# Optimization experiments

Hardware: AMD Instinct MI355X
Metric: run time of the kernel (lower is better)

Reference implementation:

```python
import jax, jax.numpy as jnp
import numpy as np

N = 50000
E = 600000
F_IN = 256
H = 128            # num_hidden_units * num_heads (heads=1)
C = 20             # num_classes
NEG_SLOPE = 0.2    # PyG GATConv default


def setup_inputs() -> dict:
    key = jax.random.key(0)
    ks = jax.random.split(key, 16)
    g = lambda k, shape, fan: jax.random.normal(k, shape, jnp.float32) / np.sqrt(fan)
    return {
        "x": jax.random.normal(ks[0], (N, F_IN), jnp.float32),
        "edge_index": jax.random.randint(ks[1], (2, E), 0, N, jnp.int64),
        # GATConv 1: F_IN -> H (heads=1, concat)
        "W1": g(ks[2], (F_IN, H), F_IN),
        "a_src1": g(ks[3], (H,), H),
        "a_dst1": g(ks[4], (H,), H),
        "b1": jnp.zeros((H,), jnp.float32),
        # GATConv 2: H -> H (heads=1)
        "W2": g(ks[5], (H, H), H),
        "a_src2": g(ks[6], (H,), H),
        "a_dst2": g(ks[7], (H,), H),
        "b2": jnp.zeros((H,), jnp.float32),
        # MLP head
        "Wm1": g(ks[8], (H, H), H),
        "bm1": jnp.zeros((H,), jnp.float32),
        "Wm2": g(ks[9], (H, C), H),
        "bm2": jnp.zeros((C,), jnp.float32),
    }


def gat_layer(x, W, a_src, a_dst, b, src, dst, n_nodes):
    """Single-head GATConv (PyG semantics, self-loops already in src/dst)."""
    h = x @ W                                    # [N, H]
    # edge attention logits: leaky_relu(a_src . h_j + a_dst . h_i)
    logits = jax.nn.leaky_relu((h @ a_src)[src] + (h @ a_dst)[dst], NEG_SLOPE)  # [Etot]
    # softmax over incoming edges per target node
    m = jax.ops.segment_max(logits, dst, num_segments=n_nodes)
    e = jnp.exp(logits - m[dst])
    denom = jax.ops.segment_sum(e, dst, num_segments=n_nodes)
    coef = e / denom[dst]                        # [Etot]
    out = jax.ops.segment_sum(coef[:, None] * h[src], dst, num_segments=n_nodes)
    return out + b


def reference(x, edge_index, W1, a_src1, a_dst1, b1, W2, a_src2, a_dst2, b2, Wm1, bm1, Wm2, bm2):
    n = x.shape[0]
    loops = jnp.arange(n, dtype=edge_index.dtype)
    src = jnp.concatenate([edge_index[0], loops])  # add self loops (GATConv default)
    dst = jnp.concatenate([edge_index[1], loops])
    h = gat_layer(x, W1, a_src1, a_dst1, b1, src, dst, n)
    h = jax.nn.relu(h)                            # dropout = identity at eval
    h = gat_layer(h, W2, a_src2, a_dst2, b2, src, dst, n)
    # MLP head: Linear -> (dropout) -> ReLU -> Linear -> sigmoid
    z = jax.nn.relu(h @ Wm1 + bm1)
    return jax.nn.sigmoid(z @ Wm2 + bm2)
```

## Files before the change

kernel.cpp:

```cpp
#include <hip/hip_runtime.h>
#include <math.h>

#define F_IN 256
#define HDIM 128
#define NCLS 20
#define NEG_SLOPE 0.2f
#define SCAN_CHUNK 1024

typedef float f32x4 __attribute__((ext_vector_type(4)));
typedef _Float16 f16x2 __attribute__((ext_vector_type(2)));
typedef _Float16 f16x4 __attribute__((ext_vector_type(4)));
typedef _Float16 f16x8 __attribute__((ext_vector_type(8)));

static __device__ __forceinline__ float lrelu(float x) { return x > 0.f ? x : NEG_SLOPE * x; }

__global__ __launch_bounds__(256) void zero_kernel(int4* __restrict__ p, int n4) {
    int i = blockIdx.x * blockDim.x + threadIdx.x;
    if (i < n4) p[i] = make_int4(0, 0, 0, 0);
}

__global__ void count_kernel(const int* __restrict__ ei, int E, int N, int* __restrict__ deg) {
    int e = blockIdx.x * blockDim.x + threadIdx.x;
    int Etot = E + N;
    if (e >= Etot) return;
    int d = (e < E) ? ei[E + e] : (e - E);
    atomicAdd(&deg[d], 1);
}

__global__ __launch_bounds__(256) void scan_reduce_kernel(const int* __restrict__ deg, int n,
                                                          int* __restrict__ bsums) {
    int base = blockIdx.x * SCAN_CHUNK + threadIdx.x * 4;
    int s = 0;
    if (base + 3 < n) {
        int4 v = *reinterpret_cast<const int4*>(&deg[base]);
        s = v.x + v.y + v.z + v.w;
    } else {
#pragma unroll
        for (int j = 0; j < 4; ++j) if (base + j < n) s += deg[base + j];
    }
#pragma unroll
    for (int o = 32; o > 0; o >>= 1) s += __shfl_down(s, o);
    __shared__ int ws[4];
    int lane = threadIdx.x & 63, w = threadIdx.x >> 6;
    if (lane == 0) ws[w] = s;
    __syncthreads();
    if (threadIdx.x == 0) bsums[blockIdx.x] = ws[0] + ws[1] + ws[2] + ws[3];
}

__global__ __launch_bounds__(256) void scan_bsums_kernel(int* __restrict__ bsums, int nb,
                                                         int* __restrict__ off, int n) {
    __shared__ int sh[256];
    int tid = threadIdx.x;
    int v = (tid < nb) ? bsums[tid] : 0;
    sh[tid] = v;
    __syncthreads();
    for (int d = 1; d < 256; d <<= 1) {
        int t = (tid >= d) ? sh[tid - d] : 0;
        __syncthreads();
        sh[tid] += t;
        __syncthreads();
    }
    if (tid < nb) bsums[tid] = sh[tid] - v;
    if (tid == 255) off[n] = sh[255];
}

__global__ __launch_bounds__(256) void scan_down_kernel(const int* __restrict__ deg, int n,
                                                        const int* __restrict__ bpre,
                                                        int* __restrict__ off) {
    int base = blockIdx.x * SCAN_CHUNK + threadIdx.x * 4;
    int v0 = 0, v1 = 0, v2 = 0, v3 = 0;
    if (base + 3 < n) {
        int4 t = *reinterpret_cast<const int4*>(&deg[base]);
        v0 = t.x; v1 = t.y; v2 = t.z; v3 = t.w;
    } else {
        if (base + 0 < n) v0 = deg[base + 0];
        if (base + 1 < n) v1 = deg[base + 1];
        if (base + 2 < n) v2 = deg[base + 2];
        if (base + 3 < n) v3 = deg[base + 3];
    }
    int tsum = v0 + v1 + v2 + v3;
    int lane = threadIdx.x & 63, w = threadIdx.x >> 6;
    int inc = tsum;
#pragma unroll
    for (int o = 1; o < 64; o <<= 1) {
        int t = __shfl_up(inc, o);
        if (lane >= o) inc += t;
    }
    int texc = inc - tsum;
    __shared__ int wsum[4];
    if (lane == 63) wsum[w] = inc;
    __syncthreads();
    int wpre = 0;
    for (int i = 0; i < w; ++i) wpre += wsum[i];
    int p = bpre[blockIdx.x] + wpre + texc;
    if (base + 3 < n) {
        int4 o4;
        o4.x = p; o4.y = p + v0; o4.z = p + v0 + v1; o4.w = p + v0 + v1 + v2;
        *reinterpret_cast<int4*>(&off[base]) = o4;
    } else {
        int run = p;
        if (base + 0 < n) { off[base + 0] = run; run += v0; }
        if (base + 1 < n) { off[base + 1] = run; run += v1; }
        if (base + 2 < n) { off[base + 2] = run; run += v2; }
        if (base + 3 < n) { off[base + 3] = run; }
    }
}

__global__ void scatter_kernel(const int* __restrict__ ei, int E, int N,
                               const int* __restrict__ off, int* __restrict__ deg,
                               int* __restrict__ csr_src) {
    int e = blockIdx.x * blockDim.x + threadIdx.x;
    int Etot = E + N;
    if (e >= Etot) return;
    int s, d;
    if (e < E) { s = ei[e]; d = ei[E + e]; } else { s = d = e - E; }
    int pos = off[d] + atomicSub(&deg[d], 1) - 1;
    csr_src[pos] = s;
}

__global__ __launch_bounds__(64) void pack_b_kernel(const float* __restrict__ W1,
                                                    const float* __restrict__ W2,
                                                    const float* __restrict__ Wm1,
                                                    _Float16* __restrict__ p1,
                                                    _Float16* __restrict__ p2,
                                                    _Float16* __restrict__ p3) {
    int t = blockIdx.x;
    int lane = threadIdx.x;
    const float* B; _Float16* out; int r;
    if (t < 64)      { B = W1;  out = p1; r = t; }
    else if (t < 96) { B = W2;  out = p2; r = t - 64; }
    else             { B = Wm1; out = p3; r = t - 96; }
    int ks = r >> 3, cf = r & 7;
    int c  = cf * 16 + (lane & 15);
    int k0 = ks * 32 + (lane >> 4) * 8;
    size_t base = ((size_t)r * 64 + lane) * 16;
#pragma unroll
    for (int i = 0; i < 8; ++i) {
        float v = B[(size_t)(k0 + i) * 128 + c];
        _Float16 h = (_Float16)v;
        out[base + i]     = h;
        out[base + 8 + i] = (_Float16)(v - (float)h);
    }
}

template <int AFMT, int KSTEPS, int FUSE_HEAD>
__global__ __launch_bounds__(256) void gemm_mfma_kernel(
        const void* __restrict__ Aptr, const _Float16* __restrict__ Bp,
        _Float16* __restrict__ C, int M,
        const float* __restrict__ bias, int act,
        const float* __restrict__ a_src, const float* __restrict__ a_dst,
        float* __restrict__ as_out, float* __restrict__ ad_out,
        const float* __restrict__ Wh, const float* __restrict__ bh2,
        float* __restrict__ outp) {
    constexpr int K = KSTEPS * 32;
    __shared__ float sal[2][2][64];
    __shared__ float zs[FUSE_HEAD ? 64 : 1][FUSE_HEAD ? 132 : 1];
    __shared__ float Wt[FUSE_HEAD ? 20 : 1][FUSE_HEAD ? 132 : 1];
    __shared__ float bb[FUSE_HEAD ? 20 : 1];

    int tid = threadIdx.x;
    int lane = tid & 63;
    int wid = tid >> 6;
    int wr = wid >> 1, wc = wid & 1;
    int bm = blockIdx.x * 64;
    int l15 = lane & 15, l4 = lane >> 4;
    int row0 = bm + wr * 32 + l15;
    int koff = l4 * 8;

    if constexpr (FUSE_HEAD) {
        for (int i = tid; i < HDIM * NCLS; i += 256) Wt[i % NCLS][i / NCLS] = Wh[i];
        if (tid < NCLS) bb[tid] = bh2[tid];
    }

    const float*    A32 = (const float*)Aptr;
    const _Float16* A16 = (const _Float16*)Aptr;
    bool ok0 = row0 < M, ok1 = (row0 + 16) < M;
    const f16x8 zf = {0, 0, 0, 0, 0, 0, 0, 0};

    f32x4 acc[2][4];
#pragma unroll
    for (int m = 0; m < 2; ++m)
#pragma unroll
        for (int j = 0; j < 4; ++j) acc[m][j] = (f32x4){0.f, 0.f, 0.f, 0.f};

    auto loadA = [&](int ks, f16x8 a[2]) {
        int kb = ks * 32 + koff;
#pragma unroll
        for (int m = 0; m < 2; ++m) {
            int rr = row0 + m * 16;
            bool ok = m ? ok1 : ok0;
            if (AFMT == 0) {
                if (ok) {
                    const float* p = &A32[(size_t)rr * K + kb];
                    float4 u = *reinterpret_cast<const float4*>(p);
                    float4 w = *reinterpret_cast<const float4*>(p + 4);
                    f16x8 t;
                    t[0] = (_Float16)u.x; t[1] = (_Float16)u.y;
                    t[2] = (_Float16)u.z; t[3] = (_Float16)u.w;
                    t[4] = (_Float16)w.x; t[5] = (_Float16)w.y;
                    t[6] = (_Float16)w.z; t[7] = (_Float16)w.w;
                    a[m] = t;
                } else a[m] = zf;
            } else {
                a[m] = ok ? *reinterpret_cast<const f16x8*>(&A16[(size_t)rr * K + kb]) : zf;
            }
        }
    };
    auto loadB = [&](int ks, f16x8 bh[4], f16x8 bl[4]) {
#pragma unroll
        for (int j = 0; j < 4; ++j) {
            int cf = wc * 4 + j;
            const _Float16* p = Bp + (((size_t)ks * 8 + cf) * 64 + lane) * 16;
            bh[j] = *reinterpret_cast<const f16x8*>(p);
            bl[j] = *reinterpret_cast<const f16x8*>(p + 8);
        }
    };

    f16x8 a0[2], a1[2], bh0[4], bh1[4], bl0[4], bl1[4];
    loadA(0, a0); loadB(0, bh0, bl0);
#pragma unroll
    for (int ks = 0; ks < KSTEPS; ks += 2) {
        loadA(ks + 1, a1); loadB(ks + 1, bh1, bl1);
#pragma unroll
        for (int j = 0; j < 4; ++j) {
            acc[0][j] = __builtin_amdgcn_mfma_f32_16x16x32_f16(a0[0], bh0[j], acc[0][j], 0, 0, 0);
            acc[1][j] = __builtin_amdgcn_mfma_f32_16x16x32_f16(a0[1], bh0[j], acc[1][j], 0, 0, 0);
            acc[0][j] = __builtin_amdgcn_mfma_f32_16x16x32_f16(a0[0], bl0[j], acc[0][j], 0, 0, 0);
            acc[1][j] = __builtin_amdgcn_mfma_f32_16x16x32_f16(a0[1], bl0[j], acc[1][j], 0, 0, 0);
        }
        if (ks + 2 < KSTEPS) { loadA(ks + 2, a0); loadB(ks + 2, bh0, bl0); }
#pragma unroll
        for (int j = 0; j < 4; ++j) {
            acc[0][j] = __builtin_amdgcn_mfma_f32_16x16x32_f16(a1[0], bh1[j], acc[0][j], 0, 0, 0);
            acc[1][j] = __builtin_amdgcn_mfma_f32_16x16x32_f16(a1[1], bh1[j], acc[1][j], 0, 0, 0);
            acc[0][j] = __builtin_amdgcn_mfma_f32_16x16x32_f16(a1[0], bl1[j], acc[0][j], 0, 0, 0);
            acc[1][j] = __builtin_amdgcn_mfma_f32_16x16x32_f16(a1[1], bl1[j], acc[1][j], 0, 0, 0);
        }
    }

    float ps[2][4], pd[2][4];
#pragma unroll
    for (int m = 0; m < 2; ++m)
#pragma unroll
        for (int reg = 0; reg < 4; ++reg) { ps[m][reg] = 0.f; pd[m][reg] = 0.f; }

#pragma unroll
    for (int j = 0; j < 4; ++j) {
        int col = wc * 64 + j * 16 + l15;
        float bi = bias ? bias[col] : 0.f;
        float asc = a_src ? a_src[col] : 0.f;
        float adc = a_src ? a_dst[col] : 0.f;
#pragma unroll
        for (int m = 0; m < 2; ++m) {
#pragma unroll
            for (int reg = 0; reg < 4; ++reg) {
                int rloc = wr * 32 + m * 16 + l4 * 4 + reg;
                int rr = bm + rloc;
                float v = acc[m][j][reg] + bi;
                if (act) v = fmaxf(v, 0.f);
                if constexpr (FUSE_HEAD) {
                    zs[rloc][col] = v;
                } else {
                    if (rr < M) C[(size_t)rr * 128 + col] = (_Float16)v;
                }
                ps[m][reg] = fmaf(v, asc, ps[m][reg]);
                pd[m][reg] = fmaf(v, adc, pd[m][reg]);
            }
        }
    }

    if (a_src) {
#pragma unroll
        for (int o = 1; o < 16; o <<= 1) {
#pragma unroll
            for (int m = 0; m < 2; ++m)
#pragma unroll
                for (int reg = 0; reg < 4; ++reg) {
                    ps[m][reg] += __shfl_xor(ps[m][reg], o);
                    pd[m][reg] += __shfl_xor(pd[m][reg], o);
                }
        }
        if (l15 == 0) {
#pragma unroll
            for (int m = 0; m < 2; ++m)
#pragma unroll
                for (int reg = 0; reg < 4; ++reg) {
                    int rloc = wr * 32 + m * 16 + l4 * 4 + reg;
                    sal[0][wc][rloc] = ps[m][reg];
                    sal[1][wc][rloc] = pd[m][reg];
                }
        }
        __syncthreads();
        if (tid < 64) {
            int rr = bm + tid;
            if (rr < M) {
                as_out[rr] = sal[0][0][tid] + sal[0][1][tid];
                ad_out[rr] = sal[1][0][tid] + sal[1][1][tid];
            }
        }
    }

    if constexpr (FUSE_HEAD) {
        __syncthreads();
        for (int idx = tid; idx < 64 * NCLS; idx += 256) {
            int r = idx / NCLS, c = idx % NCLS;
            int rr = bm + r;
            if (rr >= M) continue;
            float s = bb[c];
#pragma unroll
            for (int k = 0; k < HDIM; k += 4) {
                float4 z4 = *reinterpret_cast<const float4*>(&zs[r][k]);
                float4 w4 = *reinterpret_cast<const float4*>(&Wt[c][k]);
                s = fmaf(z4.x, w4.x, s);
                s = fmaf(z4.y, w4.y, s);
                s = fmaf(z4.z, w4.z, s);
                s = fmaf(z4.w, w4.w, s);
            }
            outp[(size_t)rr * NCLS + c] = 1.f / (1.f + __expf(-s));
        }
    }
}

__global__ __launch_bounds__(256) void aggregate_kernel(const _Float16* __restrict__ h,
                                 const float* __restrict__ asrc, const float* __restrict__ adst,
                                 const int* __restrict__ off, const int* __restrict__ csr_src,
                                 const float* __restrict__ bias,
                                 _Float16* __restrict__ out,
                                 int N, int do_relu) {
    __shared__ float2 sm[4][64];
    int wslot = threadIdx.x >> 6;
    int wave = blockIdx.x * 4 + wslot;
    int lane = threadIdx.x & 63;
    if (wave >= N) return;
    int o0 = off[wave], o1 = off[wave + 1];
    float ad = adst[wave];
    int l15 = lane & 15;
    int eslot = lane >> 4;

    float denom = 0.f;
    float acc[8];
#pragma unroll
    for (int i = 0; i < 8; ++i) acc[i] = 0.f;

    for (int base = o0; base < o1; base += 64) {
        int cnt = o1 - base; if (cnt > 64) cnt = 64;
        float e = 0.f; int s = 0;
        if (lane < cnt) {
            s = csr_src[base + lane];
            e = __expf(lrelu(asrc[s] + ad));
        }
        float t = e;
#pragma unroll
        for (int o = 32; o > 0; o >>= 1) t += __shfl_xor(t, o);
        denom += t;
        sm[wslot][lane] = make_float2(__int_as_float(s), e);
        for (int j = eslot; j < cnt; j += 4) {
            float2 se = sm[wslot][j];
            int s0 = __float_as_int(se.x);
            f16x8 hv = *reinterpret_cast<const f16x8*>(&h[(size_t)s0 * HDIM + 8 * l15]);
#pragma unroll
            for (int i = 0; i < 8; ++i) acc[i] = fmaf(se.y, (float)hv[i], acc[i]);
        }
    }

#pragma unroll
    for (int i = 0; i < 8; ++i) {
        acc[i] += __shfl_xor(acc[i], 16);
        acc[i] += __shfl_xor(acc[i], 32);
    }

    if (lane < 16) {
        float inv = 1.f / denom;
        float4 b0 = *reinterpret_cast<const float4*>(&bias[8 * l15]);
        float4 b1 = *reinterpret_cast<const float4*>(&bias[8 * l15 + 4]);
        float bv[8] = {b0.x, b0.y, b0.z, b0.w, b1.x, b1.y, b1.z, b1.w};
        f16x8 o8;
#pragma unroll
        for (int i = 0; i < 8; ++i) {
            float v = acc[i] * inv + bv[i];
            if (do_relu) v = fmaxf(v, 0.f);
            o8[i] = (_Float16)v;
        }
        *reinterpret_cast<f16x8*>(&out[(size_t)wave * HDIM + 8 * l15]) = o8;
    }
}

extern "C" void kernel_launch(void* const* d_in, const int* in_sizes, int n_in,
                              void* d_out, int out_size, void* d_ws, size_t ws_size,
                              hipStream_t stream) {
    const float* x      = (const float*)d_in[0];
    const int*   ei     = (const int*)d_in[1];
    const float* W1     = (const float*)d_in[2];
    const float* a_src1 = (const float*)d_in[3];
    const float* a_dst1 = (const float*)d_in[4];
    const float* b1     = (const float*)d_in[5];
    const float* W2     = (const float*)d_in[6];
    const float* a_src2 = (const float*)d_in[7];
    const float* a_dst2 = (const float*)d_in[8];
    const float* b2     = (const float*)d_in[9];
    const float* Wm1    = (const float*)d_in[10];
    const float* bm1    = (const float*)d_in[11];
    const float* Wm2    = (const float*)d_in[12];
    const float* bm2    = (const float*)d_in[13];

    int N = in_sizes[0] / F_IN;
    int E = in_sizes[1] / 2;
    int Etot = E + N;

    char* ws = (char*)d_ws;
    size_t pos = 0;
    auto alloc = [&](size_t bytes) -> void* {
        void* p = ws + pos;
        pos = (pos + bytes + 255) & ~(size_t)255;
        return p;
    };
    _Float16* h16 = (_Float16*)alloc((size_t)N * HDIM * 2);
    _Float16* f16 = (_Float16*)alloc((size_t)N * HDIM * 2);
    float* as_buf = (float*)alloc((size_t)N * 4);
    float* ad_buf = (float*)alloc((size_t)N * 4);
    int*   deg    = (int*)alloc((size_t)((N + 3) & ~3) * 4);
    int*   offs   = (int*)alloc((size_t)(N + 1) * 4);
    int*   csr    = (int*)alloc((size_t)Etot * 4);
    int*   bsums  = (int*)alloc(256 * 4);
    _Float16* p1 = (_Float16*)alloc(65536 * 2);
    _Float16* p2 = (_Float16*)alloc(32768 * 2);
    _Float16* p3 = (_Float16*)alloc(32768 * 2);

    int eb = (Etot + 255) / 256;
    int nb = (N + SCAN_CHUNK - 1) / SCAN_CHUNK;
    int n4 = (N + 3) / 4;

    zero_kernel<<<(n4 + 255) / 256, 256, 0, stream>>>((int4*)deg, n4);
    count_kernel<<<eb, 256, 0, stream>>>(ei, E, N, deg);
    scan_reduce_kernel<<<nb, 256, 0, stream>>>(deg, N, bsums);
    scan_bsums_kernel<<<1, 256, 0, stream>>>(bsums, nb, offs, N);
    scan_down_kernel<<<nb, 256, 0, stream>>>(deg, N, bsums, offs);
    scatter_kernel<<<eb, 256, 0, stream>>>(ei, E, N, offs, deg, csr);

    pack_b_kernel<<<128, 64, 0, stream>>>(W1, W2, Wm1, p1, p2, p3);

    int gemm_blocks = (N + 63) / 64;
    int wave_blocks = (N + 3) / 4;

    gemm_mfma_kernel<0, 8, 0><<<gemm_blocks, 256, 0, stream>>>(x, p1, h16, N, nullptr, 0,
                                                               a_src1, a_dst1, as_buf, ad_buf,
                                                               nullptr, nullptr, nullptr);
    aggregate_kernel<<<wave_blocks, 256, 0, stream>>>(h16, as_buf, ad_buf, offs, csr, b1, f16, N, 1);

    gemm_mfma_kernel<1, 4, 0><<<gemm_blocks, 256, 0, stream>>>(f16, p2, h16, N, nullptr, 0,
                                                               a_src2, a_dst2, as_buf, ad_buf,
                                                               nullptr, nullptr, nullptr);
    aggregate_kernel<<<wave_blocks, 256, 0, stream>>>(h16, as_buf, ad_buf, offs, csr, b2, f16, N, 0);

    gemm_mfma_kernel<1, 4, 1><<<gemm_blocks, 256, 0, stream>>>(f16, p3, h16, N, bm1, 1,
                                                               nullptr, nullptr, nullptr, nullptr,
                                                               Wm2, bm2, (float*)d_out);
}
```

Before: 210.7 us.

## Split GEMM K dimension across two wave groups with shared-memory reduction

Doubles the GEMM block to 512 threads. Two groups of four waves each compute half of the K reduction for the same 64x128 output tile. Group 1 writes its partial accumulators to a padded shared buffer, and group 0 adds them before running the existing epilogue (bias, activation, attention dot products, fused head). This adds latency-hiding parallelism per tile, at the cost of extra LDS traffic, an additional barrier, and a larger shared footprint that may lower occupancy.

```diff
diff --git a/kernel.cpp b/kernel.cpp
--- a/kernel.cpp
+++ b/kernel.cpp
@@ -144,7 +144,7 @@
 }
 
 template <int AFMT, int KSTEPS, int FUSE_HEAD>
-__global__ __launch_bounds__(256) void gemm_mfma_kernel(
+__global__ __launch_bounds__(512) void gemm_mfma_kernel(
         const void* __restrict__ Aptr, const _Float16* __restrict__ Bp,
         _Float16* __restrict__ C, int M,
         const float* __restrict__ bias, int act,
@@ -152,23 +152,27 @@
         float* __restrict__ as_out, float* __restrict__ ad_out,
         const float* __restrict__ Wh, const float* __restrict__ bh2,
         float* __restrict__ outp) {
-    constexpr int K = KSTEPS * 32;
+    constexpr int K  = KSTEPS * 32;
+    constexpr int HK = KSTEPS / 2;
+    __shared__ float comb[64][132];
     __shared__ float sal[2][2][64];
-    __shared__ float zs[FUSE_HEAD ? 64 : 1][FUSE_HEAD ? 132 : 1];
     __shared__ float Wt[FUSE_HEAD ? 20 : 1][FUSE_HEAD ? 132 : 1];
     __shared__ float bb[FUSE_HEAD ? 20 : 1];
 
     int tid = threadIdx.x;
     int lane = tid & 63;
     int wid = tid >> 6;
-    int wr = wid >> 1, wc = wid & 1;
+    int g   = wid >> 2;
+    int wsub = wid & 3;
+    int wr = wsub >> 1, wc = wsub & 1;
     int bm = blockIdx.x * 64;
     int l15 = lane & 15, l4 = lane >> 4;
     int row0 = bm + wr * 32 + l15;
     int koff = l4 * 8;
+    int kg = g * HK;
 
     if constexpr (FUSE_HEAD) {
-        for (int i = tid; i < HDIM * NCLS; i += 256) Wt[i % NCLS][i / NCLS] = Wh[i];
+        for (int i = tid; i < HDIM * NCLS; i += 512) Wt[i % NCLS][i / NCLS] = Wh[i];
         if (tid < NCLS) bb[tid] = bh2[tid];
     }
 
@@ -217,10 +221,10 @@
     };
 
     f16x8 a0[2], a1[2], bh0[4], bh1[4], bl0[4], bl1[4];
-    loadA(0, a0); loadB(0, bh0, bl0);
-#pragma unroll
-    for (int ks = 0; ks < KSTEPS; ks += 2) {
-        loadA(ks + 1, a1); loadB(ks + 1, bh1, bl1);
+    loadA(kg, a0); loadB(kg, bh0, bl0);
+#pragma unroll
+    for (int ks = 0; ks < HK; ks += 2) {
+        loadA(kg + ks + 1, a1); loadB(kg + ks + 1, bh1, bl1);
 #pragma unroll
         for (int j = 0; j < 4; ++j) {
             acc[0][j] = __builtin_amdgcn_mfma_f32_16x16x32_f16(a0[0], bh0[j], acc[0][j], 0, 0, 0);
@@ -228,7 +232,7 @@
             acc[0][j] = __builtin_amdgcn_mfma_f32_16x16x32_f16(a0[0], bl0[j], acc[0][j], 0, 0, 0);
             acc[1][j] = __builtin_amdgcn_mfma_f32_16x16x32_f16(a0[1], bl0[j], acc[1][j], 0, 0, 0);
         }
-        if (ks + 2 < KSTEPS) { loadA(ks + 2, a0); loadB(ks + 2, bh0, bl0); }
+        if (ks + 2 < HK) { loadA(kg + ks + 2, a0); loadB(kg + ks + 2, bh0, bl0); }
 #pragma unroll
         for (int j = 0; j < 4; ++j) {
             acc[0][j] = __builtin_amdgcn_mfma_f32_16x16x32_f16(a1[0], bh1[j], acc[0][j], 0, 0, 0);
@@ -238,78 +242,93 @@
         }
     }
 
-    float ps[2][4], pd[2][4];
-#pragma unroll
-    for (int m = 0; m < 2; ++m)
-#pragma unroll
-        for (int reg = 0; reg < 4; ++reg) { ps[m][reg] = 0.f; pd[m][reg] = 0.f; }
-
-#pragma unroll
-    for (int j = 0; j < 4; ++j) {
-        int col = wc * 64 + j * 16 + l15;
-        float bi = bias ? bias[col] : 0.f;
-        float asc = a_src ? a_src[col] : 0.f;
-        float adc = a_src ? a_dst[col] : 0.f;
-#pragma unroll
-        for (int m = 0; m < 2; ++m) {
-#pragma unroll
-            for (int reg = 0; reg < 4; ++reg) {
-                int rloc = wr * 32 + m * 16 + l4 * 4 + reg;
-                int rr = bm + rloc;
-                float v = acc[m][j][reg] + bi;
-                if (act) v = fmaxf(v, 0.f);
-                if constexpr (FUSE_HEAD) {
-                    zs[rloc][col] = v;
-                } else {
-                    if (rr < M) C[(size_t)rr * 128 + col] = (_Float16)v;
-                }
-                ps[m][reg] = fmaf(v, asc, ps[m][reg]);
-                pd[m][reg] = fmaf(v, adc, pd[m][reg]);
-            }
-        }
-    }
-
-    if (a_src) {
-#pragma unroll
-        for (int o = 1; o < 16; o <<= 1) {
+    if (g == 1) {
+#pragma unroll
+        for (int j = 0; j < 4; ++j) {
+            int col = wc * 64 + j * 16 + l15;
 #pragma unroll
             for (int m = 0; m < 2; ++m)
 #pragma unroll
-                for (int reg = 0; reg < 4; ++reg) {
-                    ps[m][reg] += __shfl_xor(ps[m][reg], o);
-                    pd[m][reg] += __shfl_xor(pd[m][reg], o);
-                }
-        }
-        if (l15 == 0) {
-#pragma unroll
-            for (int m = 0; m < 2; ++m)
+                for (int reg = 0; reg < 4; ++reg)
+                    comb[wr * 32 + m * 16 + l4 * 4 + reg][col] = acc[m][j][reg];
+        }
+    }
+    __syncthreads();
+
+    if (g == 0) {
+        float ps[2][4], pd[2][4];
+#pragma unroll
+        for (int m = 0; m < 2; ++m)
+#pragma unroll
+            for (int reg = 0; reg < 4; ++reg) { ps[m][reg] = 0.f; pd[m][reg] = 0.f; }
+
+#pragma unroll
+        for (int j = 0; j < 4; ++j) {
+            int col = wc * 64 + j * 16 + l15;
+            float bi = bias ? bias[col] : 0.f;
+            float asc = a_src ? a_src[col] : 0.f;
+            float adc = a_src ? a_dst[col] : 0.f;
+#pragma unroll
+            for (int m = 0; m < 2; ++m) {
 #pragma unroll
                 for (int reg = 0; reg < 4; ++reg) {
                     int rloc = wr * 32 + m * 16 + l4 * 4 + reg;
-                    sal[0][wc][rloc] = ps[m][reg];
-                    sal[1][wc][rloc] = pd[m][reg];
+                    int rr = bm + rloc;
+                    float v = acc[m][j][reg] + comb[rloc][col] + bi;
+                    if (act) v = fmaxf(v, 0.f);
+                    if constexpr (FUSE_HEAD) {
+                        comb[rloc][col] = v;
+                    } else {
+                        if (rr < M) C[(size_t)rr * 128 + col] = (_Float16)v;
+                    }
+                    ps[m][reg] = fmaf(v, asc, ps[m][reg]);
+                    pd[m][reg] = fmaf(v, adc, pd[m][reg]);
                 }
-        }
-        __syncthreads();
-        if (tid < 64) {
-            int rr = bm + tid;
-            if (rr < M) {
-                as_out[rr] = sal[0][0][tid] + sal[0][1][tid];
-                ad_out[rr] = sal[1][0][tid] + sal[1][1][tid];
             }
         }
+
+        if (a_src) {
+#pragma unroll
+            for (int o = 1; o < 16; o <<= 1) {
+#pragma unroll
+                for (int m = 0; m < 2; ++m)
+#pragma unroll
+                    for (int reg = 0; reg < 4; ++reg) {
+                        ps[m][reg] += __shfl_xor(ps[m][reg], o);
+                        pd[m][reg] += __shfl_xor(pd[m][reg], o);
+                    }
+            }
+            if (l15 == 0) {
+#pragma unroll
+                for (int m = 0; m < 2; ++m)
+#pragma unroll
+                    for (int reg = 0; reg < 4; ++reg) {
+                        int rloc = wr * 32 + m * 16 + l4 * 4 + reg;
+                        sal[0][wc][rloc] = ps[m][reg];
+                        sal[1][wc][rloc] = pd[m][reg];
+                    }
+            }
+        }
+    }
+    __syncthreads();
+
+    if (a_src && tid < 64) {
+        int rr = bm + tid;
+        if (rr < M) {
+            as_out[rr] = sal[0][0][tid] + sal[0][1][tid];
+            ad_out[rr] = sal[1][0][tid] + sal[1][1][tid];
+        }
     }
 
     if constexpr (FUSE_HEAD) {
-        __syncthreads();
-        for (int idx = tid; idx < 64 * NCLS; idx += 256) {
+        for (int idx = tid; idx < 64 * NCLS; idx += 512) {
             int r = idx / NCLS, c = idx % NCLS;
             int rr = bm + r;
             if (rr >= M) continue;
             float s = bb[c];
 #pragma unroll
             for (int k = 0; k < HDIM; k += 4) {
-                float4 z4 = *reinterpret_cast<const float4*>(&zs[r][k]);
+                float4 z4 = *reinterpret_cast<const float4*>(&comb[r][k]);
                 float4 w4 = *reinterpret_cast<const float4*>(&Wt[c][k]);
                 s = fmaf(z4.x, w4.x, s);
                 s = fmaf(z4.y, w4.y, s);
@@ -442,17 +461,17 @@
     int gemm_blocks = (N + 63) / 64;
     int wave_blocks = (N + 3) / 4;
 
-    gemm_mfma_kernel<0, 8, 0><<<gemm_blocks, 256, 0, stream>>>(x, p1, h16, N, nullptr, 0,
+    gemm_mfma_kernel<0, 8, 0><<<gemm_blocks, 512, 0, stream>>>(x, p1, h16, N, nullptr, 0,
                                                                a_src1, a_dst1, as_buf, ad_buf,
                                                                nullptr, nullptr, nullptr);
     aggregate_kernel<<<wave_blocks, 256, 0, stream>>>(h16, as_buf, ad_buf, offs, csr, b1, f16, N, 1);
 
-    gemm_mfma_kernel<1, 4, 0><<<gemm_blocks, 256, 0, stream>>>(f16, p2, h16, N, nullptr, 0,
+    gemm_mfma_kernel<1, 4, 0><<<gemm_blocks, 512, 0, stream>>>(f16, p2, h16, N, nullptr, 0,
                                                                a_src2, a_dst2, as_buf, ad_buf,
                                                                nullptr, nullptr, nullptr);
     aggregate_kernel<<<wave_blocks, 256, 0, stream>>>(h16, as_buf, ad_buf, offs, csr, b2, f16, N, 0);
 
-    gemm_mfma_kernel<1, 4, 1><<<gemm_blocks, 256, 0, stream>>>(f16, p3, h16, N, bm1, 1,
+    gemm_mfma_kernel<1, 4, 1><<<gemm_blocks, 512, 0, stream>>>(f16, p3, h16, N, bm1, 1,
                                                                nullptr, nullptr, nullptr, nullptr,
                                                                Wm2, bm2, (float*)d_out);
 }
```

After: 214.8 us (median of 2 runs). Within noise of the previous version (+1.9%).
